# Kernel tuning notes

Hardware: AMD Instinct MI355X
Metric: run time of the kernel (lower is better)

Reference implementation:

```python
import jax, jax.numpy as jnp
import numpy as np

NUM_AREAS = 4
NUM_TICKS = 4
AREA_N = 2048          # neurons per area
N = NUM_AREAS * AREA_N # total neurons = 8192
D_IN = 1024
N_CLASSES = 1024
BATCH = 512
THRESHOLD = 0.05


def setup_inputs() -> dict:
    key = jax.random.key(0)
    ks = jax.random.split(key, 9)
    x = jax.random.normal(ks[0], (BATCH, D_IN), jnp.float32)
    Rw = jax.random.normal(ks[1], (NUM_AREAS, AREA_N, D_IN), jnp.float32) * 0.02
    rb = jax.random.normal(ks[2], (NUM_AREAS, AREA_N), jnp.float32) * 0.02
    W_blocks = jax.random.normal(ks[3], (NUM_AREAS, NUM_AREAS, AREA_N, AREA_N), jnp.float32) * 0.02
    # bias only on diagonal blocks (in_area == out_area), else zeros, as in torch code
    b_full = jax.random.normal(ks[4], (NUM_AREAS, AREA_N), jnp.float32) * 0.02
    b_blocks = jnp.zeros((NUM_AREAS, NUM_AREAS, AREA_N), jnp.float32)
    b_blocks = b_blocks.at[jnp.arange(NUM_AREAS), jnp.arange(NUM_AREAS)].set(b_full)
    # mask init: 0.5 on diagonal blocks, 0.05 off-diagonal
    eye = jnp.eye(NUM_AREAS, dtype=jnp.float32)
    mask = (0.05 + 0.45 * eye)[:, :, None, None] * jnp.ones((NUM_AREAS, NUM_AREAS, AREA_N, AREA_N), jnp.float32)
    Ow = jax.random.normal(ks[5], (N_CLASSES, N), jnp.float32) * 0.02
    Ob = jax.random.normal(ks[6], (N_CLASSES,), jnp.float32) * 0.02
    # KMeans-like neuron partition: random permutation split into equal areas
    area_idx = jax.random.permutation(ks[7], N).reshape(NUM_AREAS, AREA_N).astype(jnp.int64)
    return {"x": x, "Rw": Rw, "rb": rb, "W_blocks": W_blocks, "b_blocks": b_blocks,
            "mask": mask, "Ow": Ow, "Ob": Ob, "area_idx": area_idx}


def reference(x, Rw, rb, W_blocks, b_blocks, mask, Ow, Ob, area_idx):
    # Initial per-area encoding: Z[a] = tanh(x @ Rw[a].T + rb[a]) -> [A, B, n]
    Z = jnp.tanh(jnp.einsum('bd,and->abn', x, Rw) + rb[:, None, :])
    history = [Z]
    # Effective masked weights (clamp mask to [0,1])
    Weff = W_blocks * jnp.clip(mask, 0.0, 1.0)  # [A_out, A_in, n_out, n_in]
    for _ in range(NUM_TICKS):
        # data-dependent skip: connection fires only if mean|Z_in| > threshold
        gate = (jnp.mean(jnp.abs(Z), axis=(1, 2)) > THRESHOLD).astype(Z.dtype)  # [A_in]
        Zg = Z * gate[:, None, None]
        Z_next = jnp.einsum('ibm,oinm->obn', Zg, Weff)
        Z_next = Z_next + jnp.einsum('i,oin->on', gate, b_blocks)[:, None, :]
        Z = jnp.tanh(Z_next)
        history.append(Z)
    B = x.shape[0]
    # Scatter per-area activations back to flat neuron order
    Zperm = jnp.transpose(Z, (1, 0, 2)).reshape(B, N)  # columns ordered as area_idx.reshape(-1)
    Z_flat = jnp.zeros((B, N), x.dtype).at[:, area_idx.reshape(-1)].set(Zperm)
    logits = Z_flat @ Ow.T + Ob
    return logits, jnp.stack(history)  # history: [T+1, A, B, n]
```

## Files before the change

kernel.cpp:

```cpp
#include <hip/hip_runtime.h>
#include <stdint.h>

typedef unsigned short u16;
typedef float floatx4 __attribute__((ext_vector_type(4)));
typedef __bf16 bf16x8 __attribute__((ext_vector_type(8)));

#define NUM_AREAS 4
#define AN 2048
#define NTOT 8192
#define BATCH 512
#define DIN 1024
#define NCLS 1024
#define THRESHOLD 0.05f
#define BAN (BATCH * AN)

__device__ __forceinline__ u16 f2bf(float f) {
    union { float f; unsigned u; } v; v.f = f;
    unsigned r = v.u + 0x7fffu + ((v.u >> 16) & 1u);
    return (u16)(r >> 16);
}

__device__ __forceinline__ void load_lds16(const u16* g, u16* l) {
    __builtin_amdgcn_global_load_lds((const __attribute__((address_space(1))) void*)g,
                                     (__attribute__((address_space(3))) void*)l,
                                     16, 0, 0);
}

__device__ __forceinline__ void gemm_tiles(const u16* __restrict__ A, int lda,
                                           const u16* __restrict__ Bm, int ldb,
                                           int klen, u16* smemA, u16* smemB,
                                           floatx4 acc[4][4]) {
    const int tid = threadIdx.x;
    const int t8 = tid * 8;
    const int lane = tid & 63;
    const int quad = lane >> 4;
    const int l15 = lane & 15;
    const int wm = ((tid >> 7) & 1) * 64;
    const int wn = ((tid >> 6) & 1) * 64;
    for (int k0 = 0; k0 < klen; k0 += 32) {
        __syncthreads();
#pragma unroll
        for (int q = 0; q < 2; ++q) {
            const int flat = q * 2048 + t8;
            const int r = flat >> 5;
            const int kk = flat & 31;
            load_lds16(A + (size_t)r * lda + (k0 + kk), smemA + flat);
            load_lds16(Bm + (size_t)r * ldb + (k0 + kk), smemB + flat);
        }
        __syncthreads();
        bf16x8 av[4], bv[4];
#pragma unroll
        for (int i = 0; i < 4; ++i)
            av[i] = *(const bf16x8*)(smemA + (wm + i * 16 + l15) * 32 + quad * 8);
#pragma unroll
        for (int i = 0; i < 4; ++i)
            bv[i] = *(const bf16x8*)(smemB + (wn + i * 16 + l15) * 32 + quad * 8);
#pragma unroll
        for (int mt = 0; mt < 4; ++mt)
#pragma unroll
            for (int nt = 0; nt < 4; ++nt)
                acc[mt][nt] = __builtin_amdgcn_mfma_f32_16x16x32_bf16(av[mt], bv[nt], acc[mt][nt], 0, 0, 0);
    }
}

__global__ void k_init(const float* __restrict__ Ob, float* __restrict__ out,
                       float* __restrict__ gacc) {
    const int i = blockIdx.x * 256 + threadIdx.x;
    if (i < BATCH * NCLS) out[i] = Ob[i & (NCLS - 1)];
    if (i < 32) gacc[i] = 0.f;
}

__global__ void k_cvt(const float* __restrict__ src, u16* __restrict__ dst, int n8) {
    const int i = blockIdx.x * 256 + threadIdx.x;
    if (i >= n8) return;
    const float4 x0 = ((const float4*)src)[2 * i];
    const float4 x1 = ((const float4*)src)[2 * i + 1];
    uint4 o;
    o.x = (unsigned)f2bf(x0.x) | ((unsigned)f2bf(x0.y) << 16);
    o.y = (unsigned)f2bf(x0.z) | ((unsigned)f2bf(x0.w) << 16);
    o.z = (unsigned)f2bf(x1.x) | ((unsigned)f2bf(x1.y) << 16);
    o.w = (unsigned)f2bf(x1.z) | ((unsigned)f2bf(x1.w) << 16);
    ((uint4*)dst)[i] = o;
}

__global__ void k_weff(const float* __restrict__ W, const float* __restrict__ mask,
                       u16* __restrict__ dst, int n8) {
    const int i = blockIdx.x * 256 + threadIdx.x;
    if (i >= n8) return;
    const float4 w0 = ((const float4*)W)[2 * i];
    const float4 w1 = ((const float4*)W)[2 * i + 1];
    const float4 m0 = ((const float4*)mask)[2 * i];
    const float4 m1 = ((const float4*)mask)[2 * i + 1];
    #define CL(m) fminf(fmaxf((m), 0.f), 1.f)
    uint4 o;
    o.x = (unsigned)f2bf(w0.x * CL(m0.x)) | ((unsigned)f2bf(w0.y * CL(m0.y)) << 16);
    o.y = (unsigned)f2bf(w0.z * CL(m0.z)) | ((unsigned)f2bf(w0.w * CL(m0.w)) << 16);
    o.z = (unsigned)f2bf(w1.x * CL(m1.x)) | ((unsigned)f2bf(w1.y * CL(m1.y)) << 16);
    o.w = (unsigned)f2bf(w1.z * CL(m1.z)) | ((unsigned)f2bf(w1.w * CL(m1.w)) << 16);
    #undef CL
    ((uint4*)dst)[i] = o;
}

__global__ void k_enc(const u16* __restrict__ xbf, const u16* __restrict__ rwbf,
                      const float* __restrict__ rb, float* __restrict__ hist0,
                      u16* __restrict__ z0, float* __restrict__ gacc) {
    __shared__ __align__(16) u16 smemA[4096];
    __shared__ __align__(16) u16 smemB[4096];
    __shared__ float red[4];
    floatx4 acc[4][4] = {};
    const int mb = blockIdx.y, nb = blockIdx.x;
    gemm_tiles(xbf + (size_t)mb * 128 * DIN, DIN,
               rwbf + (size_t)nb * 128 * DIN, DIN, DIN, smemA, smemB, acc);
    const int tid = threadIdx.x, lane = tid & 63, quad = lane >> 4, l15 = lane & 15;
    const int wm = ((tid >> 7) & 1) * 64, wn = ((tid >> 6) & 1) * 64;
    const int cbase = nb * 128;
    const int area = cbase >> 11;
    float asum = 0.f;
#pragma unroll
    for (int nt = 0; nt < 4; ++nt) {
        const int col = cbase + wn + nt * 16 + l15;
        const int n = col & (AN - 1);
        const float bias = rb[col];
#pragma unroll
        for (int mt = 0; mt < 4; ++mt) {
#pragma unroll
            for (int r = 0; r < 4; ++r) {
                const int row = mb * 128 + wm + mt * 16 + quad * 4 + r;
                const float z = tanhf(acc[mt][nt][r] + bias);
                asum += fabsf(z);
                const size_t idx = (size_t)area * BAN + (size_t)row * AN + n;
                hist0[idx] = z;
                z0[idx] = f2bf(z);
            }
        }
    }
    for (int off = 32; off > 0; off >>= 1) asum += __shfl_down(asum, off, 64);
    if (lane == 0) red[tid >> 6] = asum;
    __syncthreads();
    if (tid == 0) atomicAdd(&gacc[area], red[0] + red[1] + red[2] + red[3]);
}

__global__ void k_tick_mm(const u16* __restrict__ zprev, const u16* __restrict__ weff,
                          const float* __restrict__ gin, float* __restrict__ zacc) {
    __shared__ __align__(16) u16 smemA[4096];
    __shared__ __align__(16) u16 smemB[4096];
    const int nb = blockIdx.x, mb = blockIdx.y, i = blockIdx.z;
    const float thr = THRESHOLD * (float)BAN;
    if (!(gin[i] > thr)) return;
    floatx4 acc[4][4] = {};
    const int cbase = nb * 128;
    const int o = cbase >> 11;
    const int nbase = cbase & (AN - 1);
    gemm_tiles(zprev + (size_t)i * BAN + (size_t)mb * 128 * AN, AN,
               weff + ((size_t)(o * 4 + i) * AN + nbase) * AN, AN, AN,
               smemA, smemB, acc);
    float* __restrict__ dst = zacc + ((size_t)i * 4 + o) * BAN;
    const int tid = threadIdx.x, lane = tid & 63, quad = lane >> 4, l15 = lane & 15;
    const int wm = ((tid >> 7) & 1) * 64, wn = ((tid >> 6) & 1) * 64;
#pragma unroll
    for (int nt = 0; nt < 4; ++nt) {
        const int n = nbase + wn + nt * 16 + l15;
#pragma unroll
        for (int mt = 0; mt < 4; ++mt) {
#pragma unroll
            for (int r = 0; r < 4; ++r) {
                const int row = mb * 128 + wm + mt * 16 + quad * 4 + r;
                dst[(size_t)row * AN + n] = acc[mt][nt][r];
            }
        }
    }
}

__global__ void k_tick_ep(const float* __restrict__ zacc, const float* __restrict__ bblk,
                          const float* __restrict__ gin, float* __restrict__ hist,
                          u16* __restrict__ zcur, float* __restrict__ gout) {
    __shared__ float red[4];
    const int tid = threadIdx.x;
    const int t8 = (blockIdx.x * 256 + tid) * 8;
    const int o = t8 >> 20;
    const int n = t8 & (AN - 1);
    const int io = t8 & (BAN - 1);
    const float thr = THRESHOLD * (float)BAN;
    float s[8] = {0.f, 0.f, 0.f, 0.f, 0.f, 0.f, 0.f, 0.f};
#pragma unroll
    for (int i = 0; i < 4; ++i) {
        if (!(gin[i] > thr)) continue;
        const float4* p = (const float4*)(zacc + ((size_t)i * 4 + o) * BAN + io);
        const float4 x0 = p[0], x1 = p[1];
        const float4* bb = (const float4*)(bblk + (size_t)(o * 4 + i) * AN + n);
        const float4 b0 = bb[0], b1 = bb[1];
        s[0] += x0.x + b0.x; s[1] += x0.y + b0.y; s[2] += x0.z + b0.z; s[3] += x0.w + b0.w;
        s[4] += x1.x + b1.x; s[5] += x1.y + b1.y; s[6] += x1.z + b1.z; s[7] += x1.w + b1.w;
    }
    float asum = 0.f;
    float4 h0, h1;
    uint4 zb;
    float z0 = tanhf(s[0]), z1 = tanhf(s[1]), z2 = tanhf(s[2]), z3 = tanhf(s[3]);
    float z4 = tanhf(s[4]), z5 = tanhf(s[5]), z6 = tanhf(s[6]), z7 = tanhf(s[7]);
    asum = fabsf(z0) + fabsf(z1) + fabsf(z2) + fabsf(z3)
         + fabsf(z4) + fabsf(z5) + fabsf(z6) + fabsf(z7);
    h0.x = z0; h0.y = z1; h0.z = z2; h0.w = z3;
    h1.x = z4; h1.y = z5; h1.z = z6; h1.w = z7;
    zb.x = (unsigned)f2bf(z0) | ((unsigned)f2bf(z1) << 16);
    zb.y = (unsigned)f2bf(z2) | ((unsigned)f2bf(z3) << 16);
    zb.z = (unsigned)f2bf(z4) | ((unsigned)f2bf(z5) << 16);
    zb.w = (unsigned)f2bf(z6) | ((unsigned)f2bf(z7) << 16);
    ((float4*)(hist + t8))[0] = h0;
    ((float4*)(hist + t8))[1] = h1;
    *((uint4*)(zcur + t8)) = zb;
    for (int off = 32; off > 0; off >>= 1) asum += __shfl_down(asum, off, 64);
    if ((tid & 63) == 0) red[tid >> 6] = asum;
    __syncthreads();
    if (tid == 0) atomicAdd(&gout[o], red[0] + red[1] + red[2] + red[3]);
}

__global__ void k_scatter(const u16* __restrict__ z4, const int* __restrict__ aidx,
                          u16* __restrict__ zflat) {
    const int i = blockIdx.x * 256 + threadIdx.x;
    const int n = i & (AN - 1);
    const int bb = (i >> 11) & (BATCH - 1);
    const int a = i >> 20;
    const int j = aidx[a * AN + n];
    zflat[(size_t)bb * NTOT + j] = z4[i];
}

__global__ void k_out(const u16* __restrict__ zflat, const u16* __restrict__ owbf,
                      float* __restrict__ out) {
    __shared__ __align__(16) u16 smemA[4096];
    __shared__ __align__(16) u16 smemB[4096];
    floatx4 acc[4][4] = {};
    const int nb = blockIdx.x, mb = blockIdx.y, ks = blockIdx.z;
    gemm_tiles(zflat + (size_t)mb * 128 * NTOT + ks * 2048, NTOT,
               owbf + (size_t)nb * 128 * NTOT + ks * 2048, NTOT, 2048,
               smemA, smemB, acc);
    const int tid = threadIdx.x, lane = tid & 63, quad = lane >> 4, l15 = lane & 15;
    const int wm = ((tid >> 7) & 1) * 64, wn = ((tid >> 6) & 1) * 64;
#pragma unroll
    for (int mt = 0; mt < 4; ++mt)
#pragma unroll
        for (int nt = 0; nt < 4; ++nt)
#pragma unroll
            for (int r = 0; r < 4; ++r) {
                const int row = mb * 128 + wm + mt * 16 + quad * 4 + r;
                const int col = nb * 128 + wn + nt * 16 + l15;
                atomicAdd(&out[(size_t)row * NCLS + col], acc[mt][nt][r]);
            }
}

extern "C" void kernel_launch(void* const* d_in, const int* in_sizes, int n_in,
                              void* d_out, int out_size, void* d_ws, size_t ws_size,
                              hipStream_t stream) {
    (void)in_sizes; (void)n_in; (void)out_size; (void)ws_size;
    const float* x    = (const float*)d_in[0];
    const float* Rw   = (const float*)d_in[1];
    const float* rb   = (const float*)d_in[2];
    const float* Wb   = (const float*)d_in[3];
    const float* bblk = (const float*)d_in[4];
    const float* mask = (const float*)d_in[5];
    const float* Ow   = (const float*)d_in[6];
    const float* Ob   = (const float*)d_in[7];
    const int*   aidx = (const int*)d_in[8];

    float* out  = (float*)d_out;
    float* hist = out + (size_t)BATCH * NCLS;

    char* ws = (char*)d_ws;
    size_t off = 0;
    auto alloc = [&](size_t bytes) -> char* {
        char* p = ws + off;
        off += (bytes + 255) & ~(size_t)255;
        return p;
    };
    u16* weffbf = (u16*)alloc((size_t)16 * AN * AN * 2);
    float* zacc = (float*)alloc((size_t)16 * BAN * 4);
    u16* rwbf  = (u16*)zacc;
    u16* owbf  = (u16*)((char*)zacc + ((size_t)16 << 20));
    u16* zflat = (u16*)((char*)zacc + ((size_t)32 << 20));
    u16* xbf    = (u16*)alloc((size_t)BATCH * DIN * 2);
    u16* zb0    = (u16*)alloc((size_t)NUM_AREAS * BAN * 2);
    u16* zb1    = (u16*)alloc((size_t)NUM_AREAS * BAN * 2);
    float* gacc = (float*)alloc(32 * 4);
    u16* zb[2]  = { zb0, zb1 };

    k_init<<<(BATCH * NCLS + 255) / 256, 256, 0, stream>>>(Ob, out, gacc);
    k_cvt<<<(BATCH * DIN / 8) / 256, 256, 0, stream>>>(x, xbf, BATCH * DIN / 8);
    k_cvt<<<(NTOT * DIN / 8) / 256, 256, 0, stream>>>(Rw, rwbf, NTOT * DIN / 8);
    k_weff<<<(16 * AN * AN / 8) / 256, 256, 0, stream>>>(Wb, mask, weffbf, 16 * AN * AN / 8);

    dim3 g1(64, 4);
    k_enc<<<g1, 256, 0, stream>>>(xbf, rwbf, rb, hist, zb[0], gacc);
    dim3 gmm(64, 4, 4);
    for (int t = 1; t <= 4; ++t) {
        k_tick_mm<<<gmm, 256, 0, stream>>>(zb[(t + 1) & 1], weffbf,
                                           gacc + (t - 1) * 4, zacc);
        k_tick_ep<<<2048, 256, 0, stream>>>(zacc, bblk, gacc + (t - 1) * 4,
                                            hist + (size_t)t * NUM_AREAS * BAN,
                                            zb[t & 1], gacc + t * 4);
    }
    k_cvt<<<(NCLS * NTOT / 8) / 256, 256, 0, stream>>>(Ow, owbf, NCLS * NTOT / 8);
    k_scatter<<<(NUM_AREAS * BAN) / 256, 256, 0, stream>>>(zb[0], aidx, zflat);
    k_out<<<dim3(8, 4, 4), 256, 0, stream>>>(zflat, owbf, out);
}
```

Measured before the change: 1.126 ms.

## Double-buffer LDS staging in GEMM tiles, widen weff conversion, split k_out K further

The shared GEMM loop now double-buffers its LDS tiles: the next K slice is prefetched into the alternate buffer while MFMAs run on the current one, dropping one barrier per iteration. The aim is to overlap global-to-LDS loads with compute in the encoder, tick and output GEMMs, at the cost of doubling LDS per block, which may lower occupancy. The Weff masking kernel becomes a grid-stride loop handling 16 elements per thread with nontemporal loads and stores. The output GEMM doubles its split-K factor for more parallelism, which adds more atomic adds into the output.

New measurement: 1.138 ms. Within noise of the previous version (+1.1%).

```diff
diff --git a/kernel.cpp b/kernel.cpp
--- a/kernel.cpp
+++ b/kernel.cpp
@@ -4,6 +4,8 @@
 typedef unsigned short u16;
 typedef float floatx4 __attribute__((ext_vector_type(4)));
 typedef __bf16 bf16x8 __attribute__((ext_vector_type(8)));
+typedef float f32x4v __attribute__((ext_vector_type(4)));
+typedef unsigned u32x4v __attribute__((ext_vector_type(4)));
 
 #define NUM_AREAS 4
 #define AN 2048
@@ -26,10 +28,10 @@
                                      16, 0, 0);
 }
 
-__device__ __forceinline__ void gemm_tiles(const u16* __restrict__ A, int lda,
-                                           const u16* __restrict__ Bm, int ldb,
-                                           int klen, u16* smemA, u16* smemB,
-                                           floatx4 acc[4][4]) {
+__device__ __forceinline__ void gemm_db(const u16* __restrict__ A, int lda,
+                                        const u16* __restrict__ Bm, int ldb,
+                                        int klen, u16* sA, u16* sB,
+                                        floatx4 acc[4][4]) {
     const int tid = threadIdx.x;
     const int t8 = tid * 8;
     const int lane = tid & 63;
@@ -37,29 +39,38 @@
     const int l15 = lane & 15;
     const int wm = ((tid >> 7) & 1) * 64;
     const int wn = ((tid >> 6) & 1) * 64;
-    for (int k0 = 0; k0 < klen; k0 += 32) {
-        __syncthreads();
-#pragma unroll
-        for (int q = 0; q < 2; ++q) {
-            const int flat = q * 2048 + t8;
-            const int r = flat >> 5;
-            const int kk = flat & 31;
-            load_lds16(A + (size_t)r * lda + (k0 + kk), smemA + flat);
-            load_lds16(Bm + (size_t)r * ldb + (k0 + kk), smemB + flat);
-        }
-        __syncthreads();
+    const int r0 = t8 >> 5;
+    const int kk = t8 & 31;
+    const int nst = klen >> 5;
+
+    auto stage = [&](int buf, int k0) {
+        const int bo = buf << 12;
+        load_lds16(A + (size_t)r0 * lda + (k0 + kk), sA + bo + t8);
+        load_lds16(Bm + (size_t)r0 * ldb + (k0 + kk), sB + bo + t8);
+        load_lds16(A + (size_t)(r0 + 64) * lda + (k0 + kk), sA + bo + 2048 + t8);
+        load_lds16(Bm + (size_t)(r0 + 64) * ldb + (k0 + kk), sB + bo + 2048 + t8);
+    };
+
+    stage(0, 0);
+    __syncthreads();
+    int buf = 0;
+    for (int t = 0; t < nst; ++t) {
+        if (t + 1 < nst) stage(buf ^ 1, (t + 1) << 5);
+        const int bo = buf << 12;
         bf16x8 av[4], bv[4];
 #pragma unroll
         for (int i = 0; i < 4; ++i)
-            av[i] = *(const bf16x8*)(smemA + (wm + i * 16 + l15) * 32 + quad * 8);
+            av[i] = *(const bf16x8*)(sA + bo + (wm + i * 16 + l15) * 32 + quad * 8);
 #pragma unroll
         for (int i = 0; i < 4; ++i)
-            bv[i] = *(const bf16x8*)(smemB + (wn + i * 16 + l15) * 32 + quad * 8);
+            bv[i] = *(const bf16x8*)(sB + bo + (wn + i * 16 + l15) * 32 + quad * 8);
 #pragma unroll
         for (int mt = 0; mt < 4; ++mt)
 #pragma unroll
             for (int nt = 0; nt < 4; ++nt)
                 acc[mt][nt] = __builtin_amdgcn_mfma_f32_16x16x32_bf16(av[mt], bv[nt], acc[mt][nt], 0, 0, 0);
+        __syncthreads();
+        buf ^= 1;
     }
 }
 
@@ -84,33 +95,44 @@
 }
 
 __global__ void k_weff(const float* __restrict__ W, const float* __restrict__ mask,
-                       u16* __restrict__ dst, int n8) {
-    const int i = blockIdx.x * 256 + threadIdx.x;
-    if (i >= n8) return;
-    const float4 w0 = ((const float4*)W)[2 * i];
-    const float4 w1 = ((const float4*)W)[2 * i + 1];
-    const float4 m0 = ((const float4*)mask)[2 * i];
-    const float4 m1 = ((const float4*)mask)[2 * i + 1];
-    #define CL(m) fminf(fmaxf((m), 0.f), 1.f)
-    uint4 o;
-    o.x = (unsigned)f2bf(w0.x * CL(m0.x)) | ((unsigned)f2bf(w0.y * CL(m0.y)) << 16);
-    o.y = (unsigned)f2bf(w0.z * CL(m0.z)) | ((unsigned)f2bf(w0.w * CL(m0.w)) << 16);
-    o.z = (unsigned)f2bf(w1.x * CL(m1.x)) | ((unsigned)f2bf(w1.y * CL(m1.y)) << 16);
-    o.w = (unsigned)f2bf(w1.z * CL(m1.z)) | ((unsigned)f2bf(w1.w * CL(m1.w)) << 16);
-    #undef CL
-    ((uint4*)dst)[i] = o;
+                       u16* __restrict__ dst) {
+    const int stride = gridDim.x * 256;
+    const int n16 = (16 * AN * AN) / 16;
+    for (int i = blockIdx.x * 256 + threadIdx.x; i < n16; i += stride) {
+        const f32x4v* wp = (const f32x4v*)W + (size_t)4 * i;
+        const f32x4v* mp = (const f32x4v*)mask + (size_t)4 * i;
+        u32x4v* dp = (u32x4v*)dst + (size_t)2 * i;
+        f32x4v w[4], m[4];
+#pragma unroll
+        for (int j = 0; j < 4; ++j) w[j] = __builtin_nontemporal_load(wp + j);
+#pragma unroll
+        for (int j = 0; j < 4; ++j) m[j] = __builtin_nontemporal_load(mp + j);
+        u32x4v o[2];
+#pragma unroll
+        for (int j = 0; j < 4; ++j) {
+#pragma unroll
+            for (int k = 0; k < 4; k += 2) {
+                const float a = w[j][k] * fminf(fmaxf(m[j][k], 0.f), 1.f);
+                const float b = w[j][k + 1] * fminf(fmaxf(m[j][k + 1], 0.f), 1.f);
+                o[j >> 1][((j & 1) << 1) | (k >> 1)] =
+                    (unsigned)f2bf(a) | ((unsigned)f2bf(b) << 16);
+            }
+        }
+        __builtin_nontemporal_store(o[0], dp);
+        __builtin_nontemporal_store(o[1], dp + 1);
+    }
 }
 
 __global__ void k_enc(const u16* __restrict__ xbf, const u16* __restrict__ rwbf,
                       const float* __restrict__ rb, float* __restrict__ hist0,
                       u16* __restrict__ z0, float* __restrict__ gacc) {
-    __shared__ __align__(16) u16 smemA[4096];
-    __shared__ __align__(16) u16 smemB[4096];
+    __shared__ __align__(16) u16 smemA[8192];
+    __shared__ __align__(16) u16 smemB[8192];
     __shared__ float red[4];
     floatx4 acc[4][4] = {};
     const int mb = blockIdx.y, nb = blockIdx.x;
-    gemm_tiles(xbf + (size_t)mb * 128 * DIN, DIN,
-               rwbf + (size_t)nb * 128 * DIN, DIN, DIN, smemA, smemB, acc);
+    gemm_db(xbf + (size_t)mb * 128 * DIN, DIN,
+            rwbf + (size_t)nb * 128 * DIN, DIN, DIN, smemA, smemB, acc);
     const int tid = threadIdx.x, lane = tid & 63, quad = lane >> 4, l15 = lane & 15;
     const int wm = ((tid >> 7) & 1) * 64, wn = ((tid >> 6) & 1) * 64;
     const int cbase = nb * 128;
@@ -142,8 +164,8 @@
 
 __global__ void k_tick_mm(const u16* __restrict__ zprev, const u16* __restrict__ weff,
                           const float* __restrict__ gin, float* __restrict__ zacc) {
-    __shared__ __align__(16) u16 smemA[4096];
-    __shared__ __align__(16) u16 smemB[4096];
+    __shared__ __align__(16) u16 smemA[8192];
+    __shared__ __align__(16) u16 smemB[8192];
     const int nb = blockIdx.x, mb = blockIdx.y, i = blockIdx.z;
     const float thr = THRESHOLD * (float)BAN;
     if (!(gin[i] > thr)) return;
@@ -151,9 +173,9 @@
     const int cbase = nb * 128;
     const int o = cbase >> 11;
     const int nbase = cbase & (AN - 1);
-    gemm_tiles(zprev + (size_t)i * BAN + (size_t)mb * 128 * AN, AN,
-               weff + ((size_t)(o * 4 + i) * AN + nbase) * AN, AN, AN,
-               smemA, smemB, acc);
+    gemm_db(zprev + (size_t)i * BAN + (size_t)mb * 128 * AN, AN,
+            weff + ((size_t)(o * 4 + i) * AN + nbase) * AN, AN, AN,
+            smemA, smemB, acc);
     float* __restrict__ dst = zacc + ((size_t)i * 4 + o) * BAN;
     const int tid = threadIdx.x, lane = tid & 63, quad = lane >> 4, l15 = lane & 15;
     const int wm = ((tid >> 7) & 1) * 64, wn = ((tid >> 6) & 1) * 64;
@@ -192,13 +214,12 @@
         s[0] += x0.x + b0.x; s[1] += x0.y + b0.y; s[2] += x0.z + b0.z; s[3] += x0.w + b0.w;
         s[4] += x1.x + b1.x; s[5] += x1.y + b1.y; s[6] += x1.z + b1.z; s[7] += x1.w + b1.w;
     }
-    float asum = 0.f;
     float4 h0, h1;
     uint4 zb;
-    float z0 = tanhf(s[0]), z1 = tanhf(s[1]), z2 = tanhf(s[2]), z3 = tanhf(s[3]);
-    float z4 = tanhf(s[4]), z5 = tanhf(s[5]), z6 = tanhf(s[6]), z7 = tanhf(s[7]);
-    asum = fabsf(z0) + fabsf(z1) + fabsf(z2) + fabsf(z3)
-         + fabsf(z4) + fabsf(z5) + fabsf(z6) + fabsf(z7);
+    const float z0 = tanhf(s[0]), z1 = tanhf(s[1]), z2 = tanhf(s[2]), z3 = tanhf(s[3]);
+    const float z4 = tanhf(s[4]), z5 = tanhf(s[5]), z6 = tanhf(s[6]), z7 = tanhf(s[7]);
+    float asum = fabsf(z0) + fabsf(z1) + fabsf(z2) + fabsf(z3)
+               + fabsf(z4) + fabsf(z5) + fabsf(z6) + fabsf(z7);
     h0.x = z0; h0.y = z1; h0.z = z2; h0.w = z3;
     h1.x = z4; h1.y = z5; h1.z = z6; h1.w = z7;
     zb.x = (unsigned)f2bf(z0) | ((unsigned)f2bf(z1) << 16);
@@ -226,13 +247,13 @@
 
 __global__ void k_out(const u16* __restrict__ zflat, const u16* __restrict__ owbf,
                       float* __restrict__ out) {
-    __shared__ __align__(16) u16 smemA[4096];
-    __shared__ __align__(16) u16 smemB[4096];
+    __shared__ __align__(16) u16 smemA[8192];
+    __shared__ __align__(16) u16 smemB[8192];
     floatx4 acc[4][4] = {};
     const int nb = blockIdx.x, mb = blockIdx.y, ks = blockIdx.z;
-    gemm_tiles(zflat + (size_t)mb * 128 * NTOT + ks * 2048, NTOT,
-               owbf + (size_t)nb * 128 * NTOT + ks * 2048, NTOT, 2048,
-               smemA, smemB, acc);
+    gemm_db(zflat + (size_t)mb * 128 * NTOT + ks * 1024, NTOT,
+            owbf + (size_t)nb * 128 * NTOT + ks * 1024, NTOT, 1024,
+            smemA, smemB, acc);
     const int tid = threadIdx.x, lane = tid & 63, quad = lane >> 4, l15 = lane & 15;
     const int wm = ((tid >> 7) & 1) * 64, wn = ((tid >> 6) & 1) * 64;
 #pragma unroll
@@ -285,7 +306,7 @@
     k_init<<<(BATCH * NCLS + 255) / 256, 256, 0, stream>>>(Ob, out, gacc);
     k_cvt<<<(BATCH * DIN / 8) / 256, 256, 0, stream>>>(x, xbf, BATCH * DIN / 8);
     k_cvt<<<(NTOT * DIN / 8) / 256, 256, 0, stream>>>(Rw, rwbf, NTOT * DIN / 8);
-    k_weff<<<(16 * AN * AN / 8) / 256, 256, 0, stream>>>(Wb, mask, weffbf, 16 * AN * AN / 8);
+    k_weff<<<4096, 256, 0, stream>>>(Wb, mask, weffbf);
 
     dim3 g1(64, 4);
     k_enc<<<g1, 256, 0, stream>>>(xbf, rwbf, rb, hist, zb[0], gacc);
@@ -299,5 +320,5 @@
     }
     k_cvt<<<(NCLS * NTOT / 8) / 256, 256, 0, stream>>>(Ow, owbf, NCLS * NTOT / 8);
     k_scatter<<<(NUM_AREAS * BAN) / 256, 256, 0, stream>>>(zb[0], aidx, zflat);
-    k_out<<<dim3(8, 4, 4), 256, 0, stream>>>(zflat, owbf, out);
-}
+    k_out<<<dim3(8, 4, 8), 256, 0, stream>>>(zflat, owbf, out);
+}
```
